# Performance work log

Hardware: AMD Instinct MI355X
Metric: run time of the kernel (lower is better)

The kernel has to match this reference:

```python
import jax, jax.numpy as jnp
import numpy as np

N, E, C_IN = 100000, 800000, 128


def setup_inputs() -> dict:
    key = jax.random.key(0)
    ks = jax.random.split(key, 16)
    x = jax.random.normal(ks[0], (N, C_IN), dtype=jnp.float32)
    edge_index = jax.random.randint(ks[1], (2, E), 0, N, dtype=jnp.int64)

    def glorot(k, shape):
        lim = float(np.sqrt(6.0 / (shape[0] + shape[1])))
        return jax.random.uniform(k, shape, jnp.float32, -lim, lim)

    # channels = [128, 128, 256, 256, 256, 112]; layers 0,3 are l_GCN, layers 1,2,4 are l_SAGE
    params = dict(
        alpha=0.1 * jax.random.normal(ks[2], (5,), jnp.float32),  # ReZero alphas (init'd !=0 to exercise path)
        W0=glorot(ks[3], (128, 128)), b0=jnp.zeros((128,), jnp.float32),
        W1=glorot(ks[4], (128, 256)), R1=glorot(ks[5], (128, 256)), b1=jnp.zeros((256,), jnp.float32),
        W2=glorot(ks[6], (256, 256)), R2=glorot(ks[7], (256, 256)), b2=jnp.zeros((256,), jnp.float32),
        W3=glorot(ks[8], (256, 256)), b3=jnp.zeros((256,), jnp.float32),
        W4=glorot(ks[9], (256, 112)), R4=glorot(ks[10], (256, 112)), b4=jnp.zeros((112,), jnp.float32),
    )
    return dict(x=x, edge_index=edge_index, **params)


def reference(x, edge_index, alpha, W0, b0, W1, R1, b1, W2, R2, b2, W3, b3, W4, R4, b4):
    n = x.shape[0]
    row, col = edge_index[0], edge_index[1]
    ones = jnp.ones((row.shape[0],), x.dtype)
    deg = jax.ops.segment_sum(ones, row, num_segments=n)        # out-degree per node
    dinv = jnp.where(deg > 0, jax.lax.rsqrt(jnp.maximum(deg, 1e-12)), 0.0)
    cnt = jnp.maximum(deg, 1.0)[:, None]                        # mean-aggregation denominator

    def gcn_agg(h):  # D^-1/2 A D^-1/2 @ h
        m = h[col] * dinv[col][:, None]                          # [E, C] gather + scale
        return jax.ops.segment_sum(m, row, num_segments=n) * dinv[:, None]

    def mean_agg(h):  # SparseTensor.matmul(h, reduce='mean')
        return jax.ops.segment_sum(h[col], row, num_segments=n) / cnt

    # layer 0: l_GCN, re_list, rezero=1 -> residual from y[0]; dropout = identity (eval)
    t0 = gcn_agg(x) @ W0 + b0
    h = x + alpha[0] * t0
    # layer 1: l_SAGE + relu
    h = jax.nn.relu(mean_agg(h) @ W1 + h @ R1 + b1)
    # layer 2: l_SAGE + relu
    h = jax.nn.relu(mean_agg(h) @ W2 + h @ R2 + b2)
    # layer 3: l_GCN, re_list, rezero=1 -> residual from y[3] (current h)
    t3 = gcn_agg(h) @ W3 + b3
    h = h + alpha[3] * t3
    # layer 4: l_SAGE, no relu, no residual
    h = mean_agg(h) @ W4 + h @ R4 + b4
    return h
```

## Files before the change

### kernel.cpp

```cpp
#include <hip/hip_runtime.h>


typedef _Float16 __attribute__((ext_vector_type(8))) f16x8;
typedef _Float16 __attribute__((ext_vector_type(2))) f16x2;
typedef __attribute__((ext_vector_type(4))) float f32x4;

__device__ __forceinline__ unsigned short f2h(float f) {
    union { _Float16 h; unsigned short u; } v; v.h = (_Float16)f; return v.u;
}
__device__ __forceinline__ float h2f(unsigned short u) {
    union { unsigned short u; _Float16 h; } v; v.u = u; return (float)v.h;
}


__global__ __launch_bounds__(256) void zero_int_kernel(int* __restrict__ p, int n)
{
    int i = blockIdx.x * 256 + threadIdx.x;
    if (i < n) p[i] = 0;
}

__global__ __launch_bounds__(256) void count_deg_kernel(
    const int* __restrict__ row, int* __restrict__ deg, int E)
{
    int e = blockIdx.x * 256 + threadIdx.x;
    if (e < E) atomicAdd(&deg[row[e]], 1);
}

__global__ __launch_bounds__(1024) void scan_p1_kernel(
    const int* __restrict__ deg, int* __restrict__ rp,
    int* __restrict__ bsum, int n)
{
    __shared__ int wsum[16];
    int t = threadIdx.x, lane = t & 63, w = t >> 6;
    int base = blockIdx.x * 2048;
    int carry = 0;
    #pragma unroll
    for (int half = 0; half < 2; ++half) {
        int i = base + half * 1024 + t;
        int xv = (i < n) ? deg[i] : 0;
        int s = xv;
        #pragma unroll
        for (int off = 1; off < 64; off <<= 1) {
            int v = __shfl_up(s, off, 64);
            if (lane >= off) s += v;
        }
        if (lane == 63) wsum[w] = s;
        __syncthreads();
        if (w == 0 && lane < 16) {
            int ws = wsum[lane];
            #pragma unroll
            for (int off = 1; off < 16; off <<= 1) {
                int v = __shfl_up(ws, off, 64);
                if (lane >= off) ws += v;
            }
            wsum[lane] = ws;
        }
        __syncthreads();
        int wo = (w == 0) ? 0 : wsum[w - 1];
        if (i < n) rp[i + 1] = carry + wo + s;
        carry += wsum[15];
        if (half == 0) __syncthreads();
    }
    if (t == 0) bsum[blockIdx.x] = carry;
}

__global__ __launch_bounds__(64) void scan_p2_kernel(int* __restrict__ bsum, int B)
{
    int lane = threadIdx.x;
    int v = (lane < B) ? bsum[lane] : 0;
    int s = v;
    #pragma unroll
    for (int off = 1; off < 64; off <<= 1) {
        int u = __shfl_up(s, off, 64);
        if (lane >= off) s += u;
    }
    if (lane < B) bsum[lane] = s - v;
}

__global__ __launch_bounds__(1024) void scan_p3_kernel(
    const int* __restrict__ deg, int* __restrict__ rp,
    int* __restrict__ cursor, const int* __restrict__ bsum,
    float* __restrict__ dinv, float* __restrict__ cinv, int n)
{
    int boff = bsum[blockIdx.x];
    int base = blockIdx.x * 2048;
    #pragma unroll
    for (int half = 0; half < 2; ++half) {
        int i = base + half * 1024 + threadIdx.x;
        if (i < n) {
            int d = deg[i];
            int incl = rp[i + 1] + boff;
            rp[i + 1] = incl;
            cursor[i] = incl - d;
            float df = (float)d;
            dinv[i] = (d > 0) ? rsqrtf(df) : 0.0f;
            cinv[i] = 1.0f / fmaxf(df, 1.0f);
        }
    }
    if (blockIdx.x == 0 && threadIdx.x == 0) rp[0] = 0;
}

__global__ __launch_bounds__(256) void fill_csr_kernel(
    const int* __restrict__ row, const int* __restrict__ col,
    int* __restrict__ cursor, int* __restrict__ colS, int E)
{
    int e = blockIdx.x * 256 + threadIdx.x;
    if (e < E) {
        int p = atomicAdd(&cursor[row[e]], 1);
        colS[p] = col[e];
    }
}


__global__ __launch_bounds__(256) void f32_to_f16_kernel(
    const float* __restrict__ src, unsigned short* __restrict__ dst, int n4)
{
    int i = blockIdx.x * 256 + threadIdx.x;
    if (i >= n4) return;
    float4 v = ((const float4*)src)[i];
    ushort4 o;
    o.x = f2h(v.x); o.y = f2h(v.y); o.z = f2h(v.z); o.w = f2h(v.w);
    ((ushort4*)dst)[i] = o;
}

__global__ __launch_bounds__(256) void prep_w_kernel(
    const float* __restrict__ S1, int K1,
    const float* __restrict__ S2, int K2,
    int Nout, int Npad, unsigned short* __restrict__ dst)
{
    int Ktot = K1 + K2;
    int idx = blockIdx.x * 256 + threadIdx.x;
    if (idx >= Npad * Ktot) return;
    int n = idx / Ktot, k = idx - n * Ktot;
    float v = 0.0f;
    if (n < Nout)
        v = (k < K1) ? S1[(size_t)k * Nout + n] : S2[(size_t)(k - K1) * Nout + n];
    dst[idx] = f2h(v);
}


template <int C, bool HAS_ES>
__global__ __launch_bounds__(256) void agg_f16_kernel(
    const unsigned short* __restrict__ h, int ldh,
    const int* __restrict__ rp, const int* __restrict__ cols,
    const float* __restrict__ escale, const float* __restrict__ nscale,
    unsigned short* __restrict__ out, int ldo, int n)
{
    constexpr int LPE = (C == 256) ? 32 : 16;
    constexpr int EPG = 64 / LPE;
    constexpr int UNR = 4;
    int node = blockIdx.x * 4 + (threadIdx.x >> 6);
    if (node >= n) return;
    int lane = threadIdx.x & 63;
    int grp = lane / LPE, sub = lane % LPE;
    const unsigned short* hc = h + sub * 8;

    int s = rp[node], e = rp[node + 1];
    const _Float16 hz = (_Float16)0.0f;
    f16x2 zz = { hz, hz };
    f16x2 acc2[4];
    #pragma unroll
    for (int k = 0; k < 4; ++k) acc2[k] = zz;

    for (int i = s; i < e; i += UNR * EPG) {
        int cc[UNR]; f16x2 ssv[UNR]; uint4 uu[UNR];
        #pragma unroll
        for (int u = 0; u < UNR; ++u) {
            int ii = i + u * EPG + grp;
            bool valid = ii < e;
            int c = valid ? cols[ii] : 0;
            cc[u] = c;
            float sc = valid ? (HAS_ES ? escale[c] : 1.0f) : 0.0f;
            _Float16 sh = (_Float16)sc;
            f16x2 sv = { sh, sh };
            ssv[u] = sv;
        }
        #pragma unroll
        for (int u = 0; u < UNR; ++u)
            uu[u] = *(const uint4*)(hc + (size_t)cc[u] * ldh);
        #pragma unroll
        for (int u = 0; u < UNR; ++u) {
            union { uint4 q; f16x2 hh[4]; } cv; cv.q = uu[u];
            #pragma unroll
            for (int p = 0; p < 4; ++p)
                acc2[p] += cv.hh[p] * ssv[u];
        }
    }

    #pragma unroll
    for (int k = 0; k < 4; ++k) {
        union { f16x2 h2; float f; } a, b;
        a.h2 = acc2[k];
        if (EPG == 4) { b.f = __shfl_xor(a.f, 16, 64); a.h2 = a.h2 + b.h2; }
        b.f = __shfl_xor(a.f, 32, 64); a.h2 = a.h2 + b.h2;
        acc2[k] = a.h2;
    }

    if (grp == 0) {
        _Float16 nh = (_Float16)nscale[node];
        f16x2 nn = { nh, nh };
        union { uint4 q; f16x2 hh[4]; } o;
        #pragma unroll
        for (int p = 0; p < 4; ++p) o.hh[p] = acc2[p] * nn;
        *(uint4*)(out + (size_t)node * ldo + sub * 8) = o.q;
    }
}


__device__ __forceinline__ void g2l16(const unsigned short* g, unsigned short* l) {
    __builtin_amdgcn_global_load_lds(
        (const __attribute__((address_space(1))) unsigned int*)g,
        (__attribute__((address_space(3))) unsigned int*)l, 16, 0, 0);
}

template <int BN, int EPI, bool RES_F16, bool WF32, bool WB16>
__global__ __launch_bounds__(2 * BN) void mfma_gemm_kernel(
    const unsigned short* __restrict__ A1, int K1, int lda1,
    const unsigned short* __restrict__ A2, int K2, int lda2,
    const unsigned short* __restrict__ Bt,
    const float* __restrict__ bias,
    const void* __restrict__ res, int ldres,
    const float* __restrict__ alpha_ptr, int alpha_idx,
    float* __restrict__ outf, unsigned short* __restrict__ outb, int ldo,
    int M, int Nout)
{
    constexpr int WAVES = BN / 32;
    constexpr int AI = 256 / BN;
    __shared__ unsigned short As[2][128 * 32];
    __shared__ unsigned short Bs[2][BN * 32];
    int t = threadIdx.x;
    int m0 = blockIdx.x * 128, n0 = blockIdx.y * BN;
    int Ktot = K1 + K2;
    int w = t >> 6, lane = t & 63;
    int wm = w & 1, wn = w >> 1;
    int q = lane >> 4, l16 = lane & 15;

    int koff = (((lane & 3) ^ ((lane >> 2) & 3)) * 8);
    int rsub = lane >> 2;

    f32x4 acc[4][4];
    #pragma unroll
    for (int i = 0; i < 4; ++i)
        #pragma unroll
        for (int j = 0; j < 4; ++j)
            #pragma unroll
            for (int r = 0; r < 4; ++r) acc[i][j][r] = 0.0f;

    const int KC = Ktot >> 5;

    auto issue = [&](int kc, int p) {
        int k0 = kc * 32;
        const unsigned short* Ap; int lda, kk;
        if (k0 < K1) { Ap = A1; lda = lda1; kk = k0; }
        else         { Ap = A2; lda = lda2; kk = k0 - K1; }
        #pragma unroll
        for (int a = 0; a < AI; ++a) {
            int rb = a * 16 * WAVES + w * 16;
            int gm = m0 + rb + rsub; if (gm >= M) gm = M - 1;
            g2l16(Ap + (size_t)gm * lda + kk + koff, &As[p][rb * 32]);
        }
        #pragma unroll
        for (int b = 0; b < 2; ++b) {
            int rb = b * 16 * WAVES + w * 16;
            int gn = n0 + rb + rsub;
            g2l16(Bt + (size_t)gn * Ktot + k0 + koff, &Bs[p][rb * 32]);
        }
    };

    const int cq = (q ^ (l16 & 3)) * 8;
    const int rbA = (wm * 64 + l16) * 32 + cq;
    const int rbB = (wn * 64 + l16) * 32 + cq;

    issue(0, 0);
    if (KC > 1) issue(1, 1);

    for (int kc = 0; kc < KC; ++kc) {
        int p = kc & 1;
        int rem = KC - 1 - kc;
        if (rem >= 1) {
            if constexpr (AI == 2) asm volatile("s_waitcnt vmcnt(4)" ::: "memory");
            else                   asm volatile("s_waitcnt vmcnt(3)" ::: "memory");
        } else {
            asm volatile("s_waitcnt vmcnt(0)" ::: "memory");
        }
        __builtin_amdgcn_s_barrier();
        asm volatile("" ::: "memory");

        f16x8 af[4], bfr[4];
        #pragma unroll
        for (int i = 0; i < 4; ++i)
            af[i] = *(const f16x8*)&As[p][rbA + i * 16 * 32];
        #pragma unroll
        for (int j = 0; j < 4; ++j)
            bfr[j] = *(const f16x8*)&Bs[p][rbB + j * 16 * 32];

        asm volatile("s_waitcnt lgkmcnt(0)" ::: "memory");
        __builtin_amdgcn_s_barrier();
        asm volatile("" ::: "memory");
        if (kc + 2 < KC) issue(kc + 2, p);

        __builtin_amdgcn_s_setprio(1);
        #pragma unroll
        for (int i = 0; i < 4; ++i)
            #pragma unroll
            for (int j = 0; j < 4; ++j)
                acc[i][j] = __builtin_amdgcn_mfma_f32_16x16x32_f16(
                    bfr[j], af[i], acc[i][j], 0, 0, 0);
        __builtin_amdgcn_s_setprio(0);
    }

    float alpha = 0.0f;
    if (EPI == 2) alpha = alpha_ptr[alpha_idx];
    #pragma unroll
    for (int i = 0; i < 4; ++i) {
        int m = m0 + wm * 64 + i * 16 + l16;
        if (m >= M) continue;
        #pragma unroll
        for (int j = 0; j < 4; ++j) {
            int nb = n0 + wn * 64 + j * 16 + q * 4;
            if (nb >= Nout) continue;
            float4 bv = *(const float4*)&bias[nb];
            float v0 = acc[i][j][0] + bv.x;
            float v1 = acc[i][j][1] + bv.y;
            float v2 = acc[i][j][2] + bv.z;
            float v3 = acc[i][j][3] + bv.w;
            if (EPI == 1) {
                v0 = fmaxf(v0, 0.0f); v1 = fmaxf(v1, 0.0f);
                v2 = fmaxf(v2, 0.0f); v3 = fmaxf(v3, 0.0f);
            }
            if (EPI == 2) {
                if (RES_F16) {
                    ushort4 rr = *(const ushort4*)
                        ((const unsigned short*)res + (size_t)m * ldres + nb);
                    v0 = h2f(rr.x) + alpha * v0;
                    v1 = h2f(rr.y) + alpha * v1;
                    v2 = h2f(rr.z) + alpha * v2;
                    v3 = h2f(rr.w) + alpha * v3;
                } else {
                    float4 rr = *(const float4*)
                        ((const float*)res + (size_t)m * ldres + nb);
                    v0 = rr.x + alpha * v0;
                    v1 = rr.y + alpha * v1;
                    v2 = rr.z + alpha * v2;
                    v3 = rr.w + alpha * v3;
                }
            }
            if (WF32) {
                *(float4*)&outf[(size_t)m * ldo + nb] = make_float4(v0, v1, v2, v3);
            }
            if (WB16) {
                *(ushort4*)&outb[(size_t)m * ldo + nb] =
                    make_ushort4(f2h(v0), f2h(v1), f2h(v2), f2h(v3));
            }
        }
    }
}


extern "C" void kernel_launch(void* const* d_in, const int* in_sizes, int n_in,
                              void* d_out, int out_size, void* d_ws, size_t ws_size,
                              hipStream_t stream)
{
    const float* x      = (const float*)d_in[0];
    const int*   ei     = (const int*)d_in[1];
    const float* alpha  = (const float*)d_in[2];
    const float* W0     = (const float*)d_in[3];
    const float* b0     = (const float*)d_in[4];
    const float* W1     = (const float*)d_in[5];
    const float* R1     = (const float*)d_in[6];
    const float* b1     = (const float*)d_in[7];
    const float* W2     = (const float*)d_in[8];
    const float* R2     = (const float*)d_in[9];
    const float* b2     = (const float*)d_in[10];
    const float* W3     = (const float*)d_in[11];
    const float* b3     = (const float*)d_in[12];
    const float* W4     = (const float*)d_in[13];
    const float* R4     = (const float*)d_in[14];
    const float* b4     = (const float*)d_in[15];

    const int N = in_sizes[0] / 128;
    const int E = in_sizes[1] / 2;
    const int* row = ei;
    const int* col = ei + E;

    size_t off = 0;
    auto alloc = [&](size_t bytes) -> void* {
        void* p = (char*)d_ws + off;
        off += (bytes + 255) & ~(size_t)255;
        return p;
    };
    int*   deg    = (int*)alloc((size_t)N * 4);
    int*   rp     = (int*)alloc((size_t)(N + 1) * 4);
    int*   cursor = (int*)alloc((size_t)N * 4);
    int*   colS   = (int*)alloc((size_t)E * 4);
    int*   bsum   = (int*)alloc((size_t)64 * 4);
    float* dinv   = (float*)alloc((size_t)N * 4);
    float* cinv   = (float*)alloc((size_t)N * 4);
    unsigned short* Wt0 = (unsigned short*)alloc((size_t)128 * 128 * 2);
    unsigned short* Wt1 = (unsigned short*)alloc((size_t)256 * 256 * 2);
    unsigned short* Wt2 = (unsigned short*)alloc((size_t)256 * 512 * 2);
    unsigned short* Wt3 = (unsigned short*)alloc((size_t)256 * 256 * 2);
    unsigned short* Wt4 = (unsigned short*)alloc((size_t)128 * 512 * 2);
    unsigned short* Xb  = (unsigned short*)alloc((size_t)N * 128 * 2);
    unsigned short* Gb  = (unsigned short*)alloc((size_t)N * 256 * 2);
    unsigned short* Pb  = (unsigned short*)alloc((size_t)N * 256 * 2);
    unsigned short* Ab  = (unsigned short*)alloc((size_t)N * 256 * 2);
    unsigned short* Hb  = Xb;
    (void)ws_size;

    const int SB = (N + 2047) / 2048;
    zero_int_kernel<<<(N + 255) / 256, 256, 0, stream>>>(deg, N);
    count_deg_kernel<<<(E + 255) / 256, 256, 0, stream>>>(row, deg, E);
    scan_p1_kernel<<<SB, 1024, 0, stream>>>(deg, rp, bsum, N);
    scan_p2_kernel<<<1, 64, 0, stream>>>(bsum, SB);
    scan_p3_kernel<<<SB, 1024, 0, stream>>>(deg, rp, cursor, bsum, dinv, cinv, N);
    fill_csr_kernel<<<(E + 255) / 256, 256, 0, stream>>>(row, col, cursor, colS, E);

    f32_to_f16_kernel<<<(N * 32 + 255) / 256, 256, 0, stream>>>(x, Xb, N * 32);
    prep_w_kernel<<<(128 * 128 + 255) / 256, 256, 0, stream>>>(W0, 128, nullptr, 0, 128, 128, Wt0);
    prep_w_kernel<<<(256 * 256 + 255) / 256, 256, 0, stream>>>(W1, 128, R1, 128, 256, 256, Wt1);
    prep_w_kernel<<<(256 * 512 + 255) / 256, 256, 0, stream>>>(W2, 256, R2, 256, 256, 256, Wt2);
    prep_w_kernel<<<(256 * 256 + 255) / 256, 256, 0, stream>>>(W3, 256, nullptr, 0, 256, 256, Wt3);
    prep_w_kernel<<<(128 * 512 + 255) / 256, 256, 0, stream>>>(W4, 256, R4, 256, 112, 128, Wt4);

    dim3 aggGrid((N + 3) / 4);
    dim3 g1((N + 127) / 128, 1);

    agg_f16_kernel<128, true><<<aggGrid, 256, 0, stream>>>(Xb, 128, rp, colS, dinv, dinv, Ab, 128, N);
    mfma_gemm_kernel<128, 2, false, false, true><<<g1, 256, 0, stream>>>(
        Ab, 128, 128, nullptr, 0, 0, Wt0, b0, x, 128, alpha, 0,
        nullptr, Hb, 128, N, 128);

    agg_f16_kernel<128, false><<<aggGrid, 256, 0, stream>>>(Hb, 128, rp, colS, nullptr, cinv, Ab, 128, N);
    mfma_gemm_kernel<256, 1, false, false, true><<<g1, 512, 0, stream>>>(
        Ab, 128, 128, Hb, 128, 128, Wt1, b1, nullptr, 0, nullptr, 0,
        nullptr, Gb, 256, N, 256);

    agg_f16_kernel<256, false><<<aggGrid, 256, 0, stream>>>(Gb, 256, rp, colS, nullptr, cinv, Ab, 256, N);
    mfma_gemm_kernel<256, 1, false, false, true><<<g1, 512, 0, stream>>>(
        Ab, 256, 256, Gb, 256, 256, Wt2, b2, nullptr, 0, nullptr, 0,
        nullptr, Pb, 256, N, 256);

    agg_f16_kernel<256, true><<<aggGrid, 256, 0, stream>>>(Pb, 256, rp, colS, dinv, dinv, Ab, 256, N);
    mfma_gemm_kernel<256, 2, true, false, true><<<g1, 512, 0, stream>>>(
        Ab, 256, 256, nullptr, 0, 0, Wt3, b3, Pb, 256, alpha, 3,
        nullptr, Gb, 256, N, 256);

    agg_f16_kernel<256, false><<<aggGrid, 256, 0, stream>>>(Gb, 256, rp, colS, nullptr, cinv, Ab, 256, N);
    mfma_gemm_kernel<128, 0, false, true, false><<<g1, 256, 0, stream>>>(
        Ab, 256, 256, Gb, 256, 256, Wt4, b4, nullptr, 0, nullptr, 0,
        (float*)d_out, nullptr, 112, N, 112);
}
```

Measured before the change: 690.9 us.

## Reorder last SAGE layer to project before aggregating, shrinking gathered width

The final layer now runs the GEMM first, computing h@W4 (stored as f16 in a 128-wide buffer) and h@R4+b4 (written straight to the fp32 output) in one 224-column GEMM. A 128-channel aggregation then gathers the projected features and adds the mean into the output, so the edge gather moves 112-wide rows instead of 256-wide ones. The aggregation unroll also goes from 4 to 6, and invalid lanes now skip the feature load instead of loading row 0. Aggregating after the f16 projection changes rounding slightly.

```diff
diff --git a/kernel.cpp b/kernel.cpp
--- a/kernel.cpp
+++ b/kernel.cpp
@@ -138,17 +138,37 @@
     dst[idx] = f2h(v);
 }
 
-
-template <int C, bool HAS_ES>
+__global__ __launch_bounds__(256) void prep_w2_kernel(
+    const float* __restrict__ W4, const float* __restrict__ R4,
+    unsigned short* __restrict__ dst)
+{
+    int idx = blockIdx.x * 256 + threadIdx.x;
+    int nrow = idx >> 8, k = idx & 255;
+    float v = 0.0f;
+    if (nrow < 112)      v = W4[(size_t)k * 112 + nrow];
+    else if (nrow < 224) v = R4[(size_t)k * 112 + (nrow - 112)];
+    dst[idx] = f2h(v);
+}
+
+__global__ __launch_bounds__(256) void prep_biasP_kernel(
+    const float* __restrict__ b4, float* __restrict__ biasP)
+{
+    int i = threadIdx.x;
+    biasP[i] = (i >= 112 && i < 224) ? b4[i - 112] : 0.0f;
+}
+
+
+template <int C, bool HAS_ES, int OUT_MODE>
 __global__ __launch_bounds__(256) void agg_f16_kernel(
     const unsigned short* __restrict__ h, int ldh,
     const int* __restrict__ rp, const int* __restrict__ cols,
     const float* __restrict__ escale, const float* __restrict__ nscale,
-    unsigned short* __restrict__ out, int ldo, int n)
+    unsigned short* __restrict__ out, int ldo,
+    float* __restrict__ fout, int ldof, int n)
 {
     constexpr int LPE = (C == 256) ? 32 : 16;
     constexpr int EPG = 64 / LPE;
-    constexpr int UNR = 4;
+    constexpr int UNR = 6;
     int node = blockIdx.x * 4 + (threadIdx.x >> 6);
     if (node >= n) return;
     int lane = threadIdx.x & 63;
@@ -163,12 +183,13 @@
     for (int k = 0; k < 4; ++k) acc2[k] = zz;
 
     for (int i = s; i < e; i += UNR * EPG) {
-        int cc[UNR]; f16x2 ssv[UNR]; uint4 uu[UNR];
+        bool vv[UNR]; f16x2 ssv[UNR]; uint4 uu[UNR]; int cc[UNR];
         #pragma unroll
         for (int u = 0; u < UNR; ++u) {
             int ii = i + u * EPG + grp;
             bool valid = ii < e;
-            int c = valid ? cols[ii] : 0;
+            vv[u] = valid;
+            int c = cols[valid ? ii : s];
             cc[u] = c;
             float sc = valid ? (HAS_ES ? escale[c] : 1.0f) : 0.0f;
             _Float16 sh = (_Float16)sc;
@@ -176,8 +197,12 @@
             ssv[u] = sv;
         }
         #pragma unroll
-        for (int u = 0; u < UNR; ++u)
-            uu[u] = *(const uint4*)(hc + (size_t)cc[u] * ldh);
+        for (int u = 0; u < UNR; ++u) {
+            uint4 z = { 0u, 0u, 0u, 0u };
+            uu[u] = z;
+            if (vv[u])
+                uu[u] = *(const uint4*)(hc + (size_t)cc[u] * ldh);
+        }
         #pragma unroll
         for (int u = 0; u < UNR; ++u) {
             union { uint4 q; f16x2 hh[4]; } cv; cv.q = uu[u];
@@ -196,13 +221,32 @@
         acc2[k] = a.h2;
     }
 
-    if (grp == 0) {
-        _Float16 nh = (_Float16)nscale[node];
-        f16x2 nn = { nh, nh };
-        union { uint4 q; f16x2 hh[4]; } o;
-        #pragma unroll
-        for (int p = 0; p < 4; ++p) o.hh[p] = acc2[p] * nn;
-        *(uint4*)(out + (size_t)node * ldo + sub * 8) = o.q;
+    if (OUT_MODE == 0) {
+        if (grp == 0) {
+            _Float16 nh = (_Float16)nscale[node];
+            f16x2 nn = { nh, nh };
+            union { uint4 q; f16x2 hh[4]; } o;
+            #pragma unroll
+            for (int p = 0; p < 4; ++p) o.hh[p] = acc2[p] * nn;
+            *(uint4*)(out + (size_t)node * ldo + sub * 8) = o.q;
+        }
+    } else {
+        if (grp == 0 && sub < 14) {
+            float cs = nscale[node];
+            float* U = fout + (size_t)node * ldof + sub * 8;
+            float4 u0 = *(float4*)U;
+            float4 u1 = *(float4*)(U + 4);
+            u0.x += cs * (float)acc2[0][0];
+            u0.y += cs * (float)acc2[0][1];
+            u0.z += cs * (float)acc2[1][0];
+            u0.w += cs * (float)acc2[1][1];
+            u1.x += cs * (float)acc2[2][0];
+            u1.y += cs * (float)acc2[2][1];
+            u1.z += cs * (float)acc2[3][0];
+            u1.w += cs * (float)acc2[3][1];
+            *(float4*)U = u0;
+            *(float4*)(U + 4) = u1;
+        }
     }
 }
 
@@ -324,6 +368,16 @@
             float v1 = acc[i][j][1] + bv.y;
             float v2 = acc[i][j][2] + bv.z;
             float v3 = acc[i][j][3] + bv.w;
+            if (EPI == 3) {
+                if (nb < 112) {
+                    *(ushort4*)&outb[(size_t)m * ldo + nb] =
+                        make_ushort4(f2h(v0), f2h(v1), f2h(v2), f2h(v3));
+                } else {
+                    *(float4*)&outf[(size_t)m * ldres + (nb - 112)] =
+                        make_float4(v0, v1, v2, v3);
+                }
+                continue;
+            }
             if (EPI == 1) {
                 v0 = fmaxf(v0, 0.0f); v1 = fmaxf(v1, 0.0f);
                 v2 = fmaxf(v2, 0.0f); v3 = fmaxf(v3, 0.0f);
@@ -400,7 +454,8 @@
     unsigned short* Wt1 = (unsigned short*)alloc((size_t)256 * 256 * 2);
     unsigned short* Wt2 = (unsigned short*)alloc((size_t)256 * 512 * 2);
     unsigned short* Wt3 = (unsigned short*)alloc((size_t)256 * 256 * 2);
-    unsigned short* Wt4 = (unsigned short*)alloc((size_t)128 * 512 * 2);
+    unsigned short* Wt4p= (unsigned short*)alloc((size_t)256 * 256 * 2);
+    float* biasP  = (float*)alloc((size_t)256 * 4);
     unsigned short* Xb  = (unsigned short*)alloc((size_t)N * 128 * 2);
     unsigned short* Gb  = (unsigned short*)alloc((size_t)N * 256 * 2);
     unsigned short* Pb  = (unsigned short*)alloc((size_t)N * 256 * 2);
@@ -421,33 +476,39 @@
     prep_w_kernel<<<(256 * 256 + 255) / 256, 256, 0, stream>>>(W1, 128, R1, 128, 256, 256, Wt1);
     prep_w_kernel<<<(256 * 512 + 255) / 256, 256, 0, stream>>>(W2, 256, R2, 256, 256, 256, Wt2);
     prep_w_kernel<<<(256 * 256 + 255) / 256, 256, 0, stream>>>(W3, 256, nullptr, 0, 256, 256, Wt3);
-    prep_w_kernel<<<(128 * 512 + 255) / 256, 256, 0, stream>>>(W4, 256, R4, 256, 112, 128, Wt4);
+    prep_w2_kernel<<<(256 * 256) / 256, 256, 0, stream>>>(W4, R4, Wt4p);
+    prep_biasP_kernel<<<1, 256, 0, stream>>>(b4, biasP);
 
     dim3 aggGrid((N + 3) / 4);
     dim3 g1((N + 127) / 128, 1);
 
-    agg_f16_kernel<128, true><<<aggGrid, 256, 0, stream>>>(Xb, 128, rp, colS, dinv, dinv, Ab, 128, N);
+    agg_f16_kernel<128, true, 0><<<aggGrid, 256, 0, stream>>>(
+        Xb, 128, rp, colS, dinv, dinv, Ab, 128, nullptr, 0, N);
     mfma_gemm_kernel<128, 2, false, false, true><<<g1, 256, 0, stream>>>(
         Ab, 128, 128, nullptr, 0, 0, Wt0, b0, x, 128, alpha, 0,
         nullptr, Hb, 128, N, 128);
 
-    agg_f16_kernel<128, false><<<aggGrid, 256, 0, stream>>>(Hb, 128, rp, colS, nullptr, cinv, Ab, 128, N);
+    agg_f16_kernel<128, false, 0><<<aggGrid, 256, 0, stream>>>(
+        Hb, 128, rp, colS, nullptr, cinv, Ab, 128, nullptr, 0, N);
     mfma_gemm_kernel<256, 1, false, false, true><<<g1, 512, 0, stream>>>(
         Ab, 128, 128, Hb, 128, 128, Wt1, b1, nullptr, 0, nullptr, 0,
         nullptr, Gb, 256, N, 256);
 
-    agg_f16_kernel<256, false><<<aggGrid, 256, 0, stream>>>(Gb, 256, rp, colS, nullptr, cinv, Ab, 256, N);
+    agg_f16_kernel<256, false, 0><<<aggGrid, 256, 0, stream>>>(
+        Gb, 256, rp, colS, nullptr, cinv, Ab, 256, nullptr, 0, N);
     mfma_gemm_kernel<256, 1, false, false, true><<<g1, 512, 0, stream>>>(
         Ab, 256, 256, Gb, 256, 256, Wt2, b2, nullptr, 0, nullptr, 0,
         nullptr, Pb, 256, N, 256);
 
-    agg_f16_kernel<256, true><<<aggGrid, 256, 0, stream>>>(Pb, 256, rp, colS, dinv, dinv, Ab, 256, N);
+    agg_f16_kernel<256, true, 0><<<aggGrid, 256, 0, stream>>>(
+        Pb, 256, rp, colS, dinv, dinv, Ab, 256, nullptr, 0, N);
     mfma_gemm_kernel<256, 2, true, false, true><<<g1, 512, 0, stream>>>(
         Ab, 256, 256, nullptr, 0, 0, Wt3, b3, Pb, 256, alpha, 3,
         nullptr, Gb, 256, N, 256);
 
-    agg_f16_kernel<256, false><<<aggGrid, 256, 0, stream>>>(Gb, 256, rp, colS, nullptr, cinv, Ab, 256, N);
-    mfma_gemm_kernel<128, 0, false, true, false><<<g1, 256, 0, stream>>>(
-        Ab, 256, 256, Gb, 256, 256, Wt4, b4, nullptr, 0, nullptr, 0,
-        (float*)d_out, nullptr, 112, N, 112);
-}
+    mfma_gemm_kernel<256, 3, false, false, false><<<g1, 512, 0, stream>>>(
+        Gb, 256, 256, nullptr, 0, 0, Wt4p, biasP, nullptr, 112, nullptr, 0,
+        (float*)d_out, Ab, 128, N, 224);
+    agg_f16_kernel<128, false, 1><<<aggGrid, 256, 0, stream>>>(
+        Ab, 128, rp, colS, nullptr, cinv, nullptr, 0, (float*)d_out, 112, N);
+}
```

Measured after the change: 678.1 us. Within noise of the previous version (-1.9%).
